# Performance work log

Measured on AMD Instinct MI355X. Metric: run time of the kernel, lower is better.

Reference implementation:

```python
import jax, jax.numpy as jnp
import numpy as np

B, L, D, H = 4, 2048, 1024, 16
HD = D // H  # head_dim = 64


def setup_inputs() -> dict:
    key = jax.random.key(0)
    ks = jax.random.split(key, 12)
    s = 1.0 / np.sqrt(D)
    return {
        "Q": jax.random.normal(ks[0], (B, L, D), jnp.float32),
        "K": jax.random.normal(ks[1], (B, L, D), jnp.float32),
        "V": jax.random.normal(ks[2], (B, L, D), jnp.float32),
        "mask": jnp.ones((1, 1, L, L), dtype=bool),
        "Wq_w": jax.random.normal(ks[3], (D, D), jnp.float32) * s,
        "Wq_b": jnp.zeros((D,), jnp.float32),
        "Wk_w": jax.random.normal(ks[4], (D, D), jnp.float32) * s,
        "Wk_b": jnp.zeros((D,), jnp.float32),
        "Wv_w": jax.random.normal(ks[5], (D, D), jnp.float32) * s,
        "Wv_b": jnp.zeros((D,), jnp.float32),
        "out_w": jax.random.normal(ks[6], (D, D), jnp.float32) * s,
        "out_b": jnp.zeros((D,), jnp.float32),
    }


def _split_heads(x):
    b, l, _ = x.shape
    return x.reshape(b, l, H, HD).transpose(0, 2, 1, 3)  # [B,H,L,HD]


def reference(Q, K, V, mask, Wq_w, Wq_b, Wk_w, Wk_b, Wv_w, Wv_b, out_w, out_b):
    # torch Linear: y = x @ W.T + b
    q = _split_heads(Q @ Wq_w.T + Wq_b)
    k = _split_heads(K @ Wk_w.T + Wk_b)
    v = _split_heads(V @ Wv_w.T + Wv_b)
    scores = jnp.einsum("bhqd,bhkd->bhqk", q, k) / jnp.sqrt(jnp.float32(HD))
    scores = jnp.where(mask, scores, -jnp.inf)
    w = jax.nn.softmax(scores, axis=-1)
    o = jnp.einsum("bhqk,bhkd->bhqd", w, v)  # [B,H,L,HD]
    o = o.transpose(0, 2, 1, 3).reshape(Q.shape[0], -1, H * HD)
    return o @ out_w.T + out_b
```

## Files before the change

### kernel.cpp

```cpp
#include <hip/hip_runtime.h>


typedef __attribute__((ext_vector_type(8))) short short8;
typedef __attribute__((ext_vector_type(4))) float f32x4;
typedef unsigned short u16_t;

#define B_SZ 4
#define L_SZ 2048
#define D_SZ 1024
#define H_SZ 16
#define M_SZ (B_SZ * L_SZ)
#define K_SZ 1024

#define QSCALE 0.18033688011112042f
#define DEFER_THR 11.54f

__device__ __forceinline__ u16_t f2bf(float x) {
  union { float f; unsigned u; } v; v.f = x;
  unsigned r = v.u + 0x7fffu + ((v.u >> 16) & 1u);
  return (u16_t)(r >> 16);
}

__device__ __forceinline__ float exp2fast(float x) {
#if __has_builtin(__builtin_amdgcn_exp2f)
  return __builtin_amdgcn_exp2f(x);
#else
  return __exp2f(x);
#endif
}

__device__ __forceinline__ void gload16(const void* g, void* l) {
  __builtin_amdgcn_global_load_lds(
      (const __attribute__((address_space(1))) unsigned*)g,
      (__attribute__((address_space(3))) unsigned*)l, 16, 0, 0);
}

__device__ __forceinline__ f32x4 mfma16(short8 a, short8 b, f32x4 c) {
  return __builtin_amdgcn_mfma_f32_16x16x32_bf16(a, b, c, 0, 0, 0);
}

__device__ __forceinline__ void conv8(const float* src, u16_t* dst) {
  float4 f0 = *(const float4*)src;
  float4 f1 = *(const float4*)(src + 4);
  short8 u;
  u[0] = (short)f2bf(f0.x); u[1] = (short)f2bf(f0.y);
  u[2] = (short)f2bf(f0.z); u[3] = (short)f2bf(f0.w);
  u[4] = (short)f2bf(f1.x); u[5] = (short)f2bf(f1.y);
  u[6] = (short)f2bf(f1.z); u[7] = (short)f2bf(f1.w);
  *(short8*)dst = u;
}

__global__ void convert_w(const float* __restrict__ w0, const float* __restrict__ w1,
                          const float* __restrict__ w2, const float* __restrict__ w3,
                          u16_t* __restrict__ dst) {
  int idx = blockIdx.x * 256 + threadIdx.x;
  int which = idx >> 17;
  int rem = idx & 131071;
  const float* src = (which == 0) ? w0 : (which == 1) ? w1 : (which == 2) ? w2 : w3;
  conv8(src + (size_t)rem * 8, dst + (size_t)idx * 8);
}

__global__ void convert_a(const float* __restrict__ a0, const float* __restrict__ a1,
                          const float* __restrict__ a2, u16_t* __restrict__ dst) {
  int idx = blockIdx.x * 256 + threadIdx.x;
  int which = idx >> 20;
  int rem = idx & 1048575;
  const float* src = (which == 0) ? a0 : (which == 1) ? a1 : a2;
  conv8(src + (size_t)rem * 8, dst + (size_t)idx * 8);
}

template<int EPI>
__global__ __launch_bounds__(256, 2)
void gemm_k(const u16_t* __restrict__ Abf, const u16_t* __restrict__ Bw,
            const float* __restrict__ bias, void* __restrict__ Cout, float scale) {
  __shared__ alignas(16) u16_t lA[128 * 64];
  __shared__ alignas(16) u16_t lB[128 * 64];
  const int tid = threadIdx.x;
  const int l = tid & 63, w = tid >> 6;
  const int wr = w >> 1, wc = w & 1;
  const int lin = blockIdx.x;
  const int nw = (lin & 7) * 64 + (lin >> 3);
  const int m0 = (nw >> 3) * 128, n0 = (nw & 7) * 128;

  float bvs[4];
#pragma unroll
  for (int nf = 0; nf < 4; ++nf) bvs[nf] = bias[n0 + wc * 64 + nf * 16 + (l & 15)] * scale;

  f32x4 acc[4][4];
#pragma unroll
  for (int a = 0; a < 4; ++a)
#pragma unroll
    for (int b = 0; b < 4; ++b) { f32x4 z = {0.f, 0.f, 0.f, 0.f}; acc[a][b] = z; }

  for (int kt = 0; kt < K_SZ / 64; ++kt) {
    const int k0 = kt * 64;
#pragma unroll
    for (int it = 0; it < 4; ++it) {
      int c = it * 256 + tid;
      int row = c >> 3;
      int kb = ((((c & 7) << 4)) ^ ((row & 7) << 4)) >> 1;
      gload16(Bw + (size_t)(n0 + row) * K_SZ + k0 + kb, (char*)lB + c * 16);
      gload16(Abf + (size_t)(m0 + row) * K_SZ + k0 + kb, (char*)lA + c * 16);
    }
    __syncthreads();
#pragma unroll
    for (int ksb = 0; ksb < 2; ++ksb) {
      const int colB = ksb * 64 + ((l >> 4) << 4);
      short8 af[4], bfr[4];
#pragma unroll
      for (int mf = 0; mf < 4; ++mf) {
        int row = wr * 64 + mf * 16 + (l & 15);
        af[mf] = *(const short8*)((const char*)lA + row * 128 + (colB ^ ((row & 7) << 4)));
      }
#pragma unroll
      for (int nf = 0; nf < 4; ++nf) {
        int row = wc * 64 + nf * 16 + (l & 15);
        bfr[nf] = *(const short8*)((const char*)lB + row * 128 + (colB ^ ((row & 7) << 4)));
      }
#pragma unroll
      for (int mf = 0; mf < 4; ++mf)
#pragma unroll
        for (int nf = 0; nf < 4; ++nf)
          acc[mf][nf] = mfma16(af[mf], bfr[nf], acc[mf][nf]);
    }
    __syncthreads();
  }
#pragma unroll
  for (int mf = 0; mf < 4; ++mf)
#pragma unroll
    for (int nf = 0; nf < 4; ++nf)
#pragma unroll
      for (int r = 0; r < 4; ++r) {
        int m = m0 + wr * 64 + mf * 16 + ((l >> 4) << 2) + r;
        int n = n0 + wc * 64 + nf * 16 + (l & 15);
        float val = fmaf(acc[mf][nf][r], scale, bvs[nf]);
        if (EPI == 0) {
          u16_t* q = (u16_t*)Cout;
          size_t idx = ((size_t)((m >> 11) * H_SZ + (n >> 6)) * L_SZ + (m & 2047)) * 64 + (n & 63);
          q[idx] = f2bf(val);
        } else if (EPI == 1) {
          u16_t* vt = (u16_t*)Cout;
          size_t idx = ((size_t)((m >> 11) * H_SZ + (n >> 6)) * 64 + (n & 63)) * L_SZ + (m & 2047);
          vt[idx] = f2bf(val);
        } else {
          ((float*)Cout)[(size_t)m * D_SZ + n] = val;
        }
      }
}

__global__ __launch_bounds__(256, 2)
void attn_k(const u16_t* __restrict__ qbuf, const u16_t* __restrict__ kbuf,
            const u16_t* __restrict__ vtbuf, u16_t* __restrict__ obuf) {
  __shared__ alignas(16) u16_t lK[2][64 * 64];
  __shared__ alignas(16) u16_t lV[2][64 * 64];
  __shared__ alignas(16) u16_t lP[4][16 * 64];
  const int tid = threadIdx.x;
  const int l = tid & 63, w = tid >> 6;
  const int lin = blockIdx.x;
  const int nw = (lin & 7) * 256 + (lin >> 3);
  const int qb0 = nw & 31, h = (nw >> 5) & 15, b = nw >> 9;
  const int bh = b * H_SZ + h;

  const int tok = qb0 * 64 + w * 16 + (l & 15);
  const u16_t* qrow = qbuf + ((size_t)bh * L_SZ + tok) * 64;
  short8 qf0 = *(const short8*)(qrow + ((l >> 4) << 3));
  short8 qf1 = *(const short8*)(qrow + 32 + ((l >> 4) << 3));

  f32x4 oacc[4];
#pragma unroll
  for (int nd = 0; nd < 4; ++nd) { f32x4 z = {0.f, 0.f, 0.f, 0.f}; oacc[nd] = z; }
  float mrun[4] = {-INFINITY, -INFINITY, -INFINITY, -INFINITY};
  float lpart[4] = {0.f, 0.f, 0.f, 0.f};

  const u16_t* kbase = kbuf + (size_t)bh * L_SZ * 64;
  const u16_t* vtbase = vtbuf + (size_t)bh * 64 * L_SZ;
  const int colB0 = (l >> 4) << 4;

  auto STAGE = [&](int buf, int kt) {
    const u16_t* ks_ = kbase + kt * 4096;
    const u16_t* vs_ = vtbase + kt * 64;
#pragma unroll
    for (int it = 0; it < 2; ++it) {
      int c = it * 256 + tid;
      int row = c >> 3;
      int kb = ((((c & 7) << 4)) ^ ((row & 7) << 4)) >> 1;
      gload16(ks_ + row * 64 + kb, (char*)lK[buf] + c * 16);
      gload16(vs_ + (size_t)row * L_SZ + kb, (char*)lV[buf] + c * 16);
    }
  };

  STAGE(0, 0);
  const int NT = L_SZ / 64;
  for (int kt = 0; kt < NT; ++kt) {
    const int cur = kt & 1;
    __syncthreads();
    if (kt + 1 < NT) STAGE(cur ^ 1, kt + 1);

    const char* Kb = (const char*)lK[cur];
    const char* Vb = (const char*)lV[cur];

    f32x4 s[4];
    __builtin_amdgcn_s_setprio(1);
#pragma unroll
    for (int nf = 0; nf < 4; ++nf) {
      int rk = nf * 16 + (l & 15);
      const char* kr = Kb + rk * 128;
      short8 k0 = *(const short8*)(kr + (colB0 ^ ((rk & 7) << 4)));
      short8 k1 = *(const short8*)(kr + ((64 + colB0) ^ ((rk & 7) << 4)));
      f32x4 z = {0.f, 0.f, 0.f, 0.f};
      z = mfma16(qf0, k0, z);
      s[nf] = mfma16(qf1, k1, z);
    }
    __builtin_amdgcn_s_setprio(0);

    float pm[4];
#pragma unroll
    for (int r = 0; r < 4; ++r) {
      pm[r] = fmaxf(fmaxf(s[0][r], s[1][r]), fmaxf(s[2][r], s[3][r]));
#pragma unroll
      for (int d2 = 1; d2 < 16; d2 <<= 1) pm[r] = fmaxf(pm[r], __shfl_xor(pm[r], d2));
    }
    int need = (pm[0] > mrun[0] + DEFER_THR) | (pm[1] > mrun[1] + DEFER_THR) |
               (pm[2] > mrun[2] + DEFER_THR) | (pm[3] > mrun[3] + DEFER_THR);
    if (__any(need)) {
#pragma unroll
      for (int r = 0; r < 4; ++r) {
        float mn = fmaxf(mrun[r], pm[r]);
        float sf = exp2fast(mrun[r] - mn);
        mrun[r] = mn;
        lpart[r] *= sf;
#pragma unroll
        for (int nd = 0; nd < 4; ++nd) oacc[nd][r] *= sf;
      }
    }
    u16_t* wp = lP[w];
#pragma unroll
    for (int nf = 0; nf < 4; ++nf)
#pragma unroll
      for (int r = 0; r < 4; ++r) {
        float p = exp2fast(s[nf][r] - mrun[r]);
        lpart[r] += p;
        int prow = ((l >> 4) << 2) + r;
        int pcb = (nf * 16 + (l & 15)) * 2;
        union { float f; unsigned u; } cv; cv.f = p;
        *(u16_t*)((char*)wp + prow * 128 + (pcb ^ ((prow & 7) << 4))) =
            (u16_t)((cv.u + 0x8000u) >> 16);
      }
    __builtin_amdgcn_s_setprio(1);
#pragma unroll
    for (int ksb = 0; ksb < 2; ++ksb) {
      int colB = ksb * 64 + colB0;
      int prow = l & 15;
      short8 pa = *(const short8*)((const char*)wp + prow * 128 + (colB ^ ((prow & 7) << 4)));
#pragma unroll
      for (int nd = 0; nd < 4; ++nd) {
        int rv = nd * 16 + (l & 15);
        short8 vf = *(const short8*)(Vb + rv * 128 + (colB ^ ((rv & 7) << 4)));
        oacc[nd] = mfma16(pa, vf, oacc[nd]);
      }
    }
    __builtin_amdgcn_s_setprio(0);
  }
  float lr[4];
#pragma unroll
  for (int r = 0; r < 4; ++r) {
    lr[r] = lpart[r];
#pragma unroll
    for (int d2 = 1; d2 < 16; d2 <<= 1) lr[r] += __shfl_xor(lr[r], d2);
    lr[r] = 1.0f / lr[r];
  }
#pragma unroll
  for (int nd = 0; nd < 4; ++nd)
#pragma unroll
    for (int r = 0; r < 4; ++r) {
      int t2 = qb0 * 64 + w * 16 + ((l >> 4) << 2) + r;
      obuf[((size_t)b * L_SZ + t2) * D_SZ + h * 64 + nd * 16 + (l & 15)] =
          f2bf(oacc[nd][r] * lr[r]);
    }
}

extern "C" void kernel_launch(void* const* d_in, const int* in_sizes, int n_in,
                              void* d_out, int out_size, void* d_ws, size_t ws_size,
                              hipStream_t stream) {
  const float* Q   = (const float*)d_in[0];
  const float* Kin = (const float*)d_in[1];
  const float* V   = (const float*)d_in[2];
  const float* Wq  = (const float*)d_in[4];
  const float* Wqb = (const float*)d_in[5];
  const float* Wk  = (const float*)d_in[6];
  const float* Wkb = (const float*)d_in[7];
  const float* Wv  = (const float*)d_in[8];
  const float* Wvb = (const float*)d_in[9];
  const float* Wo  = (const float*)d_in[10];
  const float* Wob = (const float*)d_in[11];

  char* ws = (char*)d_ws;
  const size_t MB = 1ull << 20;
  u16_t* Wqbf = (u16_t*)(ws + 0 * MB);
  u16_t* Wkbf = (u16_t*)(ws + 2 * MB);
  u16_t* Wvbf = (u16_t*)(ws + 4 * MB);
  u16_t* Wobf = (u16_t*)(ws + 6 * MB);
  u16_t* Abf  = (u16_t*)(ws + 8 * MB);
  u16_t* Qbf  = Abf;
  u16_t* Kbf  = (u16_t*)(ws + 24 * MB);
  u16_t* Vbf  = (u16_t*)(ws + 40 * MB);
  u16_t* qb   = (u16_t*)(ws + 56 * MB);
  u16_t* kb   = (u16_t*)(ws + 8 * MB);
  u16_t* vtb  = (u16_t*)(ws + 24 * MB);
  u16_t* ob   = (u16_t*)(ws + 40 * MB);

  convert_w<<<2048, 256, 0, stream>>>(Wq, Wk, Wv, Wo, (u16_t*)ws);
  convert_a<<<12288, 256, 0, stream>>>(Q, Kin, V, Abf);

  gemm_k<0><<<512, 256, 0, stream>>>(Qbf, Wqbf, Wqb, qb, QSCALE);
  gemm_k<0><<<512, 256, 0, stream>>>(Kbf, Wkbf, Wkb, kb, 1.0f);
  gemm_k<1><<<512, 256, 0, stream>>>(Vbf, Wvbf, Wvb, vtb, 1.0f);

  attn_k<<<2048, 256, 0, stream>>>(qb, kb, vtb, ob);

  gemm_k<2><<<512, 256, 0, stream>>>(ob, Wobf, Wob, (float*)d_out, 1.0f);
}
```

Baseline: 409.3 us.

## Fuse QKV projections into one GEMM launch and transpose attention MFMA layout

Merges the three Q/K/V projection GEMMs into a single 1536-block launch that picks the weight, bias and output layout per tile, with launch bounds raised to 3 waves per SIMD. The attention kernel swaps MFMA operand order so each lane owns one query row, which turns the per-row max/sum reductions into two shuffles, removes per-element shuffle loops, and packs P and output stores into 8-byte bf16 writes. K and V^T scratch now live in the output buffer to free workspace. Aliasing scratch with d_out is safe only because gemm_o writes d_out after attention has finished reading it.

```diff
diff --git a/kernel.cpp b/kernel.cpp
--- a/kernel.cpp
+++ b/kernel.cpp
@@ -19,6 +19,11 @@
   union { float f; unsigned u; } v; v.f = x;
   unsigned r = v.u + 0x7fffu + ((v.u >> 16) & 1u);
   return (u16_t)(r >> 16);
+}
+
+__device__ __forceinline__ unsigned bfpack(float a, float b) {
+  union { float f; unsigned u; } x, y; x.f = a; y.f = b;
+  return ((x.u + 0x8000u) >> 16) | ((y.u + 0x8000u) & 0xffff0000u);
 }
 
 __device__ __forceinline__ float exp2fast(float x) {
@@ -69,10 +74,94 @@
   conv8(src + (size_t)rem * 8, dst + (size_t)idx * 8);
 }
 
-template<int EPI>
+__global__ __launch_bounds__(256, 3)
+void gemm_qkv(const u16_t* __restrict__ Abf, const u16_t* __restrict__ Wall,
+              const float* __restrict__ bq, const float* __restrict__ bk,
+              const float* __restrict__ bv,
+              u16_t* __restrict__ qb, u16_t* __restrict__ kb, u16_t* __restrict__ vtb) {
+  __shared__ alignas(16) u16_t lA[128 * 64];
+  __shared__ alignas(16) u16_t lB[128 * 64];
+  const int tid = threadIdx.x;
+  const int l = tid & 63, w = tid >> 6;
+  const int wr = w >> 1, wc = w & 1;
+  const int lin = blockIdx.x;
+  const int nw = (lin & 7) * 192 + (lin >> 3);
+  const int np = nw >> 6, mp = nw & 63;
+  const int which = np >> 3;
+  const int m0 = mp * 128;
+  const int nW0 = np * 128;
+  const int n0 = (np & 7) * 128;
+  const float scale = (which == 0) ? QSCALE : 1.0f;
+  const float* bias = (which == 0) ? bq : (which == 1) ? bk : bv;
+  const u16_t* Asel = Abf + (size_t)which * ((size_t)M_SZ * K_SZ);
+
+  float bvs[4];
+#pragma unroll
+  for (int nf = 0; nf < 4; ++nf) bvs[nf] = bias[n0 + wc * 64 + nf * 16 + (l & 15)] * scale;
+
+  f32x4 acc[4][4];
+#pragma unroll
+  for (int a = 0; a < 4; ++a)
+#pragma unroll
+    for (int b = 0; b < 4; ++b) { f32x4 z = {0.f, 0.f, 0.f, 0.f}; acc[a][b] = z; }
+
+  for (int kt = 0; kt < K_SZ / 64; ++kt) {
+    const int k0 = kt * 64;
+#pragma unroll
+    for (int it = 0; it < 4; ++it) {
+      int c = it * 256 + tid;
+      int row = c >> 3;
+      int kb_ = ((((c & 7) << 4)) ^ ((row & 7) << 4)) >> 1;
+      gload16(Wall + (size_t)(nW0 + row) * K_SZ + k0 + kb_, (char*)lB + c * 16);
+      gload16(Asel + (size_t)(m0 + row) * K_SZ + k0 + kb_, (char*)lA + c * 16);
+    }
+    __syncthreads();
+#pragma unroll
+    for (int ksb = 0; ksb < 2; ++ksb) {
+      const int colB = ksb * 64 + ((l >> 4) << 4);
+      short8 af[4], bfr[4];
+#pragma unroll
+      for (int mf = 0; mf < 4; ++mf) {
+        int row = wr * 64 + mf * 16 + (l & 15);
+        af[mf] = *(const short8*)((const char*)lA + row * 128 + (colB ^ ((row & 7) << 4)));
+      }
+#pragma unroll
+      for (int nf = 0; nf < 4; ++nf) {
+        int row = wc * 64 + nf * 16 + (l & 15);
+        bfr[nf] = *(const short8*)((const char*)lB + row * 128 + (colB ^ ((row & 7) << 4)));
+      }
+#pragma unroll
+      for (int mf = 0; mf < 4; ++mf)
+#pragma unroll
+        for (int nf = 0; nf < 4; ++nf)
+          acc[mf][nf] = mfma16(af[mf], bfr[nf], acc[mf][nf]);
+    }
+    __syncthreads();
+  }
+#pragma unroll
+  for (int mf = 0; mf < 4; ++mf)
+#pragma unroll
+    for (int nf = 0; nf < 4; ++nf)
+#pragma unroll
+      for (int r = 0; r < 4; ++r) {
+        int m = m0 + wr * 64 + mf * 16 + ((l >> 4) << 2) + r;
+        int n = n0 + wc * 64 + nf * 16 + (l & 15);
+        float val = fmaf(acc[mf][nf][r], scale, bvs[nf]);
+        int bb = m >> 11, tok = m & 2047, h = n >> 6, d = n & 63;
+        if (which == 2) {
+          size_t idx = ((size_t)(bb * H_SZ + h) * 64 + d) * L_SZ + tok;
+          vtb[idx] = f2bf(val);
+        } else {
+          u16_t* dst = (which == 0) ? qb : kb;
+          size_t idx = ((size_t)(bb * H_SZ + h) * L_SZ + tok) * 64 + d;
+          dst[idx] = f2bf(val);
+        }
+      }
+}
+
 __global__ __launch_bounds__(256, 2)
-void gemm_k(const u16_t* __restrict__ Abf, const u16_t* __restrict__ Bw,
-            const float* __restrict__ bias, void* __restrict__ Cout, float scale) {
+void gemm_o(const u16_t* __restrict__ Abf, const u16_t* __restrict__ Bw,
+            const float* __restrict__ bias, float* __restrict__ Cout) {
   __shared__ alignas(16) u16_t lA[128 * 64];
   __shared__ alignas(16) u16_t lB[128 * 64];
   const int tid = threadIdx.x;
@@ -84,7 +173,7 @@
 
   float bvs[4];
 #pragma unroll
-  for (int nf = 0; nf < 4; ++nf) bvs[nf] = bias[n0 + wc * 64 + nf * 16 + (l & 15)] * scale;
+  for (int nf = 0; nf < 4; ++nf) bvs[nf] = bias[n0 + wc * 64 + nf * 16 + (l & 15)];
 
   f32x4 acc[4][4];
 #pragma unroll
@@ -133,18 +222,7 @@
       for (int r = 0; r < 4; ++r) {
         int m = m0 + wr * 64 + mf * 16 + ((l >> 4) << 2) + r;
         int n = n0 + wc * 64 + nf * 16 + (l & 15);
-        float val = fmaf(acc[mf][nf][r], scale, bvs[nf]);
-        if (EPI == 0) {
-          u16_t* q = (u16_t*)Cout;
-          size_t idx = ((size_t)((m >> 11) * H_SZ + (n >> 6)) * L_SZ + (m & 2047)) * 64 + (n & 63);
-          q[idx] = f2bf(val);
-        } else if (EPI == 1) {
-          u16_t* vt = (u16_t*)Cout;
-          size_t idx = ((size_t)((m >> 11) * H_SZ + (n >> 6)) * 64 + (n & 63)) * L_SZ + (m & 2047);
-          vt[idx] = f2bf(val);
-        } else {
-          ((float*)Cout)[(size_t)m * D_SZ + n] = val;
-        }
+        Cout[(size_t)m * D_SZ + n] = acc[mf][nf][r] + bvs[nf];
       }
 }
 
@@ -156,25 +234,24 @@
   __shared__ alignas(16) u16_t lP[4][16 * 64];
   const int tid = threadIdx.x;
   const int l = tid & 63, w = tid >> 6;
+  const int q = l & 15, g = l >> 4;
   const int lin = blockIdx.x;
   const int nw = (lin & 7) * 256 + (lin >> 3);
   const int qb0 = nw & 31, h = (nw >> 5) & 15, b = nw >> 9;
   const int bh = b * H_SZ + h;
 
-  const int tok = qb0 * 64 + w * 16 + (l & 15);
+  const int tok = qb0 * 64 + w * 16 + q;
   const u16_t* qrow = qbuf + ((size_t)bh * L_SZ + tok) * 64;
-  short8 qf0 = *(const short8*)(qrow + ((l >> 4) << 3));
-  short8 qf1 = *(const short8*)(qrow + 32 + ((l >> 4) << 3));
+  short8 qf0 = *(const short8*)(qrow + 8 * g);
+  short8 qf1 = *(const short8*)(qrow + 32 + 8 * g);
 
   f32x4 oacc[4];
 #pragma unroll
   for (int nd = 0; nd < 4; ++nd) { f32x4 z = {0.f, 0.f, 0.f, 0.f}; oacc[nd] = z; }
-  float mrun[4] = {-INFINITY, -INFINITY, -INFINITY, -INFINITY};
-  float lpart[4] = {0.f, 0.f, 0.f, 0.f};
+  float mrun = -INFINITY, lpart = 0.f;
 
   const u16_t* kbase = kbuf + (size_t)bh * L_SZ * 64;
   const u16_t* vtbase = vtbuf + (size_t)bh * 64 * L_SZ;
-  const int colB0 = (l >> 4) << 4;
 
   auto STAGE = [&](int buf, int kt) {
     const u16_t* ks_ = kbase + kt * 4096;
@@ -189,6 +266,9 @@
     }
   };
 
+  char* wpb = (char*)lP[w] + q * 128;
+  const int swz = (q & 7) << 4;
+
   STAGE(0, 0);
   const int NT = L_SZ / 64;
   for (int kt = 0; kt < NT; ++kt) {
@@ -203,80 +283,72 @@
     __builtin_amdgcn_s_setprio(1);
 #pragma unroll
     for (int nf = 0; nf < 4; ++nf) {
-      int rk = nf * 16 + (l & 15);
+      int rk = nf * 16 + q;
       const char* kr = Kb + rk * 128;
-      short8 k0 = *(const short8*)(kr + (colB0 ^ ((rk & 7) << 4)));
-      short8 k1 = *(const short8*)(kr + ((64 + colB0) ^ ((rk & 7) << 4)));
+      short8 k0 = *(const short8*)(kr + ((16 * g) ^ ((rk & 7) << 4)));
+      short8 k1 = *(const short8*)(kr + ((64 + 16 * g) ^ ((rk & 7) << 4)));
       f32x4 z = {0.f, 0.f, 0.f, 0.f};
-      z = mfma16(qf0, k0, z);
-      s[nf] = mfma16(qf1, k1, z);
+      z = mfma16(k0, qf0, z);
+      s[nf] = mfma16(k1, qf1, z);
     }
     __builtin_amdgcn_s_setprio(0);
 
-    float pm[4];
-#pragma unroll
-    for (int r = 0; r < 4; ++r) {
-      pm[r] = fmaxf(fmaxf(s[0][r], s[1][r]), fmaxf(s[2][r], s[3][r]));
-#pragma unroll
-      for (int d2 = 1; d2 < 16; d2 <<= 1) pm[r] = fmaxf(pm[r], __shfl_xor(pm[r], d2));
-    }
-    int need = (pm[0] > mrun[0] + DEFER_THR) | (pm[1] > mrun[1] + DEFER_THR) |
-               (pm[2] > mrun[2] + DEFER_THR) | (pm[3] > mrun[3] + DEFER_THR);
-    if (__any(need)) {
-#pragma unroll
-      for (int r = 0; r < 4; ++r) {
-        float mn = fmaxf(mrun[r], pm[r]);
-        float sf = exp2fast(mrun[r] - mn);
-        mrun[r] = mn;
-        lpart[r] *= sf;
-#pragma unroll
-        for (int nd = 0; nd < 4; ++nd) oacc[nd][r] *= sf;
-      }
-    }
-    u16_t* wp = lP[w];
-#pragma unroll
-    for (int nf = 0; nf < 4; ++nf)
-#pragma unroll
-      for (int r = 0; r < 4; ++r) {
-        float p = exp2fast(s[nf][r] - mrun[r]);
-        lpart[r] += p;
-        int prow = ((l >> 4) << 2) + r;
-        int pcb = (nf * 16 + (l & 15)) * 2;
-        union { float f; unsigned u; } cv; cv.f = p;
-        *(u16_t*)((char*)wp + prow * 128 + (pcb ^ ((prow & 7) << 4))) =
-            (u16_t)((cv.u + 0x8000u) >> 16);
-      }
+    float pm0 = fmaxf(fmaxf(s[0][0], s[0][1]), fmaxf(s[0][2], s[0][3]));
+    float pm1 = fmaxf(fmaxf(s[1][0], s[1][1]), fmaxf(s[1][2], s[1][3]));
+    float pm2 = fmaxf(fmaxf(s[2][0], s[2][1]), fmaxf(s[2][2], s[2][3]));
+    float pm3 = fmaxf(fmaxf(s[3][0], s[3][1]), fmaxf(s[3][2], s[3][3]));
+    float pm = fmaxf(fmaxf(pm0, pm1), fmaxf(pm2, pm3));
+    pm = fmaxf(pm, __shfl_xor(pm, 16));
+    pm = fmaxf(pm, __shfl_xor(pm, 32));
+
+    if (__any(pm > mrun + DEFER_THR)) {
+      float mn = fmaxf(mrun, pm);
+      float sf = exp2fast(mrun - mn);
+      mrun = mn;
+      lpart *= sf;
+#pragma unroll
+      for (int nd = 0; nd < 4; ++nd)
+#pragma unroll
+        for (int r = 0; r < 4; ++r) oacc[nd][r] *= sf;
+    }
+
+#pragma unroll
+    for (int nf = 0; nf < 4; ++nf) {
+      float p0 = exp2fast(s[nf][0] - mrun);
+      float p1 = exp2fast(s[nf][1] - mrun);
+      float p2 = exp2fast(s[nf][2] - mrun);
+      float p3 = exp2fast(s[nf][3] - mrun);
+      lpart += (p0 + p1) + (p2 + p3);
+      uint2 uu; uu.x = bfpack(p0, p1); uu.y = bfpack(p2, p3);
+      *(uint2*)(wpb + ((32 * nf + 8 * g) ^ swz)) = uu;
+    }
+
     __builtin_amdgcn_s_setprio(1);
 #pragma unroll
     for (int ksb = 0; ksb < 2; ++ksb) {
-      int colB = ksb * 64 + colB0;
-      int prow = l & 15;
-      short8 pa = *(const short8*)((const char*)wp + prow * 128 + (colB ^ ((prow & 7) << 4)));
+      int colB = ksb * 64 + 16 * g;
+      short8 pb = *(const short8*)(wpb + (colB ^ swz));
 #pragma unroll
       for (int nd = 0; nd < 4; ++nd) {
-        int rv = nd * 16 + (l & 15);
+        int rv = nd * 16 + q;
         short8 vf = *(const short8*)(Vb + rv * 128 + (colB ^ ((rv & 7) << 4)));
-        oacc[nd] = mfma16(pa, vf, oacc[nd]);
+        oacc[nd] = mfma16(vf, pb, oacc[nd]);
       }
     }
     __builtin_amdgcn_s_setprio(0);
   }
-  float lr[4];
-#pragma unroll
-  for (int r = 0; r < 4; ++r) {
-    lr[r] = lpart[r];
-#pragma unroll
-    for (int d2 = 1; d2 < 16; d2 <<= 1) lr[r] += __shfl_xor(lr[r], d2);
-    lr[r] = 1.0f / lr[r];
+
+  lpart += __shfl_xor(lpart, 16);
+  lpart += __shfl_xor(lpart, 32);
+  float lr = 1.0f / lpart;
+  u16_t* orow = obuf + ((size_t)b * L_SZ + tok) * D_SZ + h * 64;
+#pragma unroll
+  for (int nd = 0; nd < 4; ++nd) {
+    uint2 uu;
+    uu.x = bfpack(oacc[nd][0] * lr, oacc[nd][1] * lr);
+    uu.y = bfpack(oacc[nd][2] * lr, oacc[nd][3] * lr);
+    *(uint2*)(orow + nd * 16 + 4 * g) = uu;
   }
-#pragma unroll
-  for (int nd = 0; nd < 4; ++nd)
-#pragma unroll
-    for (int r = 0; r < 4; ++r) {
-      int t2 = qb0 * 64 + w * 16 + ((l >> 4) << 2) + r;
-      obuf[((size_t)b * L_SZ + t2) * D_SZ + h * 64 + nd * 16 + (l & 15)] =
-          f2bf(oacc[nd][r] * lr[r]);
-    }
 }
 
 extern "C" void kernel_launch(void* const* d_in, const int* in_sizes, int n_in,
@@ -296,27 +368,20 @@
 
   char* ws = (char*)d_ws;
   const size_t MB = 1ull << 20;
-  u16_t* Wqbf = (u16_t*)(ws + 0 * MB);
-  u16_t* Wkbf = (u16_t*)(ws + 2 * MB);
-  u16_t* Wvbf = (u16_t*)(ws + 4 * MB);
+  u16_t* Wall = (u16_t*)(ws + 0 * MB);
   u16_t* Wobf = (u16_t*)(ws + 6 * MB);
   u16_t* Abf  = (u16_t*)(ws + 8 * MB);
-  u16_t* Qbf  = Abf;
-  u16_t* Kbf  = (u16_t*)(ws + 24 * MB);
-  u16_t* Vbf  = (u16_t*)(ws + 40 * MB);
   u16_t* qb   = (u16_t*)(ws + 56 * MB);
-  u16_t* kb   = (u16_t*)(ws + 8 * MB);
-  u16_t* vtb  = (u16_t*)(ws + 24 * MB);
-  u16_t* ob   = (u16_t*)(ws + 40 * MB);
-
-  convert_w<<<2048, 256, 0, stream>>>(Wq, Wk, Wv, Wo, (u16_t*)ws);
+  u16_t* kb   = (u16_t*)d_out;
+  u16_t* vtb  = (u16_t*)d_out + 8388608;
+  u16_t* ob   = (u16_t*)(ws + 8 * MB);
+
+  convert_w<<<2048, 256, 0, stream>>>(Wq, Wk, Wv, Wo, Wall);
   convert_a<<<12288, 256, 0, stream>>>(Q, Kin, V, Abf);
 
-  gemm_k<0><<<512, 256, 0, stream>>>(Qbf, Wqbf, Wqb, qb, QSCALE);
-  gemm_k<0><<<512, 256, 0, stream>>>(Kbf, Wkbf, Wkb, kb, 1.0f);
-  gemm_k<1><<<512, 256, 0, stream>>>(Vbf, Wvbf, Wvb, vtb, 1.0f);
+  gemm_qkv<<<1536, 256, 0, stream>>>(Abf, Wall, Wqb, Wkb, Wvb, qb, kb, vtb);
 
   attn_k<<<2048, 256, 0, stream>>>(qb, kb, vtb, ob);
 
-  gemm_k<2><<<512, 256, 0, stream>>>(ob, Wobf, Wob, (float*)d_out, 1.0f);
-}
+  gemm_o<<<512, 256, 0, stream>>>(ob, Wobf, Wob, (float*)d_out);
+}
```

Result: slower. 430.5 us (+5.2%).
